# Performance work log

Measured on AMD Instinct MI355X. Metric: run time of the kernel, lower is better.

The kernel has to match this reference:

```python
import jax, jax.numpy as jnp
import numpy as np

B, S, IN = 4, 4096, 2048
E, D, A, R = 16, 128, 128, 4  # num_experts, expert_vector_dim, attn_dim, mlp_rank
LN_EPS = 1e-5


def _ln2(x, g, b):
    # LayerNorm over the last two dims [E, D] jointly (torch nn.LayerNorm([E, D]))
    mu = x.mean(axis=(-2, -1), keepdims=True)
    var = ((x - mu) ** 2).mean(axis=(-2, -1), keepdims=True)
    return (x - mu) * jax.lax.rsqrt(var + LN_EPS) * g + b


def setup_inputs() -> dict:
    key = jax.random.key(0)
    ks = jax.random.split(key, 8)
    f32 = jnp.float32
    return {
        "hidden_states": jax.random.normal(ks[0], (B, S, IN), f32),
        "expert_embedding": jax.random.normal(ks[1], (E, D), f32) * 0.02,
        "ln_gamma": jnp.ones((E, D), f32),
        "ln_beta": jnp.zeros((E, D), f32),
        "Wv_w": jax.random.normal(ks[2], (E, IN), f32) * 0.02,
        "Wv_b": jnp.zeros((E,), f32),
        "mlp_w1": jax.random.normal(ks[3], (R, IN), f32) * 0.02,
        "mlp_b1": jnp.zeros((R,), f32),
        "mlp_w2": jax.random.normal(ks[4], (E * D, R), f32) * 0.02,
        "mlp_b2": jnp.zeros((E * D,), f32),
        "te_Wq": jax.random.normal(ks[5], (A, D), f32) * 0.05,
        "te_Wk": jax.random.normal(ks[6], (A, D), f32) * 0.05,
        "top_k": 2,
    }


def reference(hidden_states, expert_embedding, ln_gamma, ln_beta, Wv_w, Wv_b,
              mlp_w1, mlp_b1, mlp_w2, mlp_b2, te_Wq, te_Wk, top_k):
    # global expert vectors, layernormed over [E, D]: (E, D)
    ge = _ln2(expert_embedding[None, None], ln_gamma, ln_beta)[0, 0]
    # input gate = W_v(hidden): (B, S, E)
    input_gate = jnp.einsum('bsi,ei->bse', hidden_states, Wv_w) + Wv_b
    # TE mlp -> dynamic per-token expert vectors: (B, S, E, D)
    h = jax.nn.relu(jnp.einsum('bsi,ri->bsr', hidden_states, mlp_w1) + mlp_b1)
    dyn = (jnp.einsum('bsr,or->bso', h, mlp_w2) + mlp_b2).reshape(B, S, E, D)
    dyn = _ln2(dyn, ln_gamma, ln_beta)
    # attention-style routing: Q from dyn experts, K from global experts
    q = jnp.einsum('bsed,ad->bsea', dyn, te_Wq)     # (B, S, E, A)
    k = jnp.einsum('ed,ad->ea', ge, te_Wk)          # (E, A)
    scale = 1.0 / float(np.sqrt(A))
    sim = jax.nn.softmax(jnp.einsum('bsqa,ka->bsqk', q, k) * scale, axis=-1)
    gate = jnp.einsum('bsqk,bsk->bsq', sim, input_gate)
    rw = jax.nn.softmax(gate, axis=-1)              # (B, S, E)
    # top-k masking + sharpened softmax (temperature 0.1)
    vals, idx = jax.lax.top_k(rw, top_k)            # (B, S, k)
    oh = jax.nn.one_hot(idx, E, dtype=rw.dtype)     # (B, S, k, E)
    scattered = jnp.einsum('bske,bsk->bse', oh, vals)
    keep = oh.sum(axis=-2) > 0
    neg = jnp.finfo(rw.dtype).min
    masked = jnp.where(keep, scattered, neg)
    return jax.nn.softmax(masked / 0.1, axis=-1)
```

## Files before the change

kernel.cpp:

```cpp
#include <hip/hip_runtime.h>
#include <math.h>

#define NTOK   16384
#define INDIM  2048
#define NROWS  20
#define CHUNK  256

#define WS_PKT  0
#define WS_D1K  1024
#define WS_GQK  1280
#define WS_BQK  1536
#define WS_SCAL 1792
#define WS_TOT  1818

#define SIM_SCALE 0.08838834764831845f

#define LBUF1   5120
#define HBUF0   10240
#define HBUF1   14336
#define LRED2_STRIDE 324
#define LRED    5440

__device__ __forceinline__ void async16(const float* g, float* l) {
    __builtin_amdgcn_global_load_lds(
        (const __attribute__((address_space(1))) void*)g,
        (__attribute__((address_space(3))) void*)l, 16, 0, 0);
}

__device__ __forceinline__ void stage_all(const float* __restrict__ wv,
                                          const float* __restrict__ w1,
                                          const float* __restrict__ hb_lane,
                                          float* ldsw, float* ldsh,
                                          int wave, int lane, int goff) {
    const int l4 = lane << 2;
    #pragma unroll
    for (int j = 0; j < 5; ++j) {
        const int r = wave + (j << 2);
        const float* src = (j < 4) ? (wv + (r << 11)) : (w1 + ((r - 16) << 11));
        async16(src + goff + l4, ldsw + r * CHUNK + l4);
    }
    #pragma unroll
    for (int t = 0; t < 4; ++t) {
        async16(hb_lane + t * INDIM + goff,
                ldsh + (((wave << 2) + t) * CHUNK) + l4);
    }
}

__device__ __forceinline__ void compute_chunk(float acc[NROWS][4],
                                              const float* wb,
                                              const float* hbl) {
    float4 h[4];
    #pragma unroll
    for (int t = 0; t < 4; ++t) h[t] = *(const float4*)(hbl + (t << 8));
    #pragma unroll
    for (int w = 0; w < NROWS; ++w) {
        float4 wf = *(const float4*)(wb + (w << 8));
        #pragma unroll
        for (int t = 0; t < 4; ++t) {
            acc[w][t] = fmaf(h[t].x, wf.x,
                        fmaf(h[t].y, wf.y,
                        fmaf(h[t].z, wf.z,
                        fmaf(h[t].w, wf.w, acc[w][t]))));
        }
    }
}

__global__ __launch_bounds__(256) void hr_pre2(
    const float* __restrict__ ee, const float* __restrict__ gam,
    const float* __restrict__ bta, const float* __restrict__ w2,
    const float* __restrict__ b2, const float* __restrict__ wq,
    const float* __restrict__ wk, float* __restrict__ ws)
{
    const int tid  = threadIdx.x;
    const int bx   = blockIdx.x;
    const int lane = tid & 63;
    const int wave = tid >> 6;

    if (bx == 16) {
        __shared__ float sacc[26];
        if (tid < 26) sacc[tid] = 0.f;
        __syncthreads();
        float pa[26];
        #pragma unroll
        for (int j = 0; j < 26; ++j) pa[j] = 0.f;
        for (int i = tid; i < 2048; i += 256) {
            float b = b2[i];
            float4 w4 = *(const float4*)(w2 + i * 4);
            float wr[4] = {w4.x, w4.y, w4.z, w4.w};
            pa[0] += b;
            pa[1] += b * b;
            #pragma unroll
            for (int r = 0; r < 4; ++r) {
                pa[2 + r] += wr[r];
                pa[6 + r] += b * wr[r];
                #pragma unroll
                for (int r2 = 0; r2 < 4; ++r2) pa[10 + r * 4 + r2] += wr[r] * wr[r2];
            }
        }
        #pragma unroll
        for (int j = 0; j < 26; ++j) {
            float v = pa[j];
            v += __shfl_xor(v, 32); v += __shfl_xor(v, 16); v += __shfl_xor(v, 8);
            v += __shfl_xor(v, 4);  v += __shfl_xor(v, 2);  v += __shfl_xor(v, 1);
            if (lane == 0) atomicAdd(&sacc[j], v);
        }
        __syncthreads();
        if (tid < 26) ws[WS_SCAL + tid] = sacc[tid] * (1.f / 2048.f);
        return;
    }

    const int e2 = bx;
    __shared__ float sge[128];
    __shared__ float sK[128];
    __shared__ float sWqK[128];
    __shared__ float sred[8];

    float v8[8];
    float s = 0.f;
    #pragma unroll
    for (int j = 0; j < 8; ++j) { v8[j] = ee[tid + j * 256]; s += v8[j]; }
    s += __shfl_xor(s, 32); s += __shfl_xor(s, 16); s += __shfl_xor(s, 8);
    s += __shfl_xor(s, 4);  s += __shfl_xor(s, 2);  s += __shfl_xor(s, 1);
    if (lane == 0) sred[wave] = s;
    __syncthreads();
    const float mu = (sred[0] + sred[1] + sred[2] + sred[3]) * (1.f / 2048.f);
    float q = 0.f;
    #pragma unroll
    for (int j = 0; j < 8; ++j) { float d = v8[j] - mu; q += d * d; }
    q += __shfl_xor(q, 32); q += __shfl_xor(q, 16); q += __shfl_xor(q, 8);
    q += __shfl_xor(q, 4);  q += __shfl_xor(q, 2);  q += __shfl_xor(q, 1);
    if (lane == 0) sred[4 + wave] = q;
    __syncthreads();
    const float rsq = rsqrtf((sred[4] + sred[5] + sred[6] + sred[7]) * (1.f / 2048.f) + 1e-5f);

    if (tid < 128) {
        int idx = (e2 << 7) + tid;
        sge[tid] = (ee[idx] - mu) * rsq * gam[idx] + bta[idx];
    }
    __syncthreads();

    {
        int a = tid >> 1, half = tid & 1;
        const float* wr = wk + (a << 7) + (half << 6);
        const float* gg = sge + (half << 6);
        float acc = 0.f;
        #pragma unroll 8
        for (int j = 0; j < 64; ++j) acc = fmaf(gg[j], wr[j], acc);
        acc += __shfl_xor(acc, 1);
        if (half == 0) sK[a] = acc;
    }
    __syncthreads();

    {
        int d = tid >> 1, half = tid & 1;
        float acc = 0.f;
        #pragma unroll 8
        for (int j = 0; j < 64; ++j) {
            int a = (half << 6) + j;
            acc = fmaf(wq[(a << 7) + d], sK[a], acc);
        }
        acc += __shfl_xor(acc, 1);
        if (half == 0) sWqK[d] = acc;
    }
    __syncthreads();

    {
        int o = tid >> 2, qd = tid & 3;
        int r = o >> 4, e = o & 15;
        float acc = 0.f;
        #pragma unroll 8
        for (int j = 0; j < 32; ++j) {
            int d  = (qd << 5) + j;
            int ed = (e << 7) + d;
            acc = fmaf(w2[ed * 4 + r] * gam[ed], sWqK[d], acc);
        }
        acc += __shfl_xor(acc, 1);
        acc += __shfl_xor(acc, 2);
        if (qd == 0) ws[WS_PKT + (e2 << 6) + (r << 4) + e] = acc;
    }

    if (tid < 192) {
        int kind = tid >> 6;
        int e    = (tid >> 2) & 15;
        int qd   = tid & 3;
        float acc = 0.f;
        #pragma unroll 8
        for (int j = 0; j < 32; ++j) {
            int d  = (qd << 5) + j;
            int ed = (e << 7) + d;
            float w = sWqK[d];
            float t = (kind == 0) ? b2[ed] * gam[ed]
                    : (kind == 1) ? gam[ed]
                                  : bta[ed];
            acc = fmaf(t, w, acc);
        }
        acc += __shfl_xor(acc, 1);
        acc += __shfl_xor(acc, 2);
        if (qd == 0) ws[WS_D1K + (kind << 8) + (e2 << 4) + e] = acc;
    }
}

__global__ __launch_bounds__(256) void hr_main(
    const float* __restrict__ hidden, const float* __restrict__ wv,
    const float* __restrict__ wvb, const float* __restrict__ w1,
    const float* __restrict__ b1, const float* __restrict__ tab,
    float* __restrict__ out)
{
    __shared__ float lds[18432];

    const int tid  = threadIdx.x;
    const int wave = tid >> 6;
    const int lane = tid & 63;
    const int tok0 = (blockIdx.x << 4) + (wave << 2);
    const float* hb = hidden + (size_t)tok0 * INDIM + (lane << 2);

    float acc[NROWS][4];
    #pragma unroll
    for (int w = 0; w < NROWS; ++w) {
        acc[w][0] = 0.f; acc[w][1] = 0.f; acc[w][2] = 0.f; acc[w][3] = 0.f;
    }

    const float* wr0 = &lds[lane << 2];
    const float* wr1 = &lds[LBUF1 + (lane << 2)];
    const float* hr0 = &lds[HBUF0 + (wave << 10) + (lane << 2)];
    const float* hr1 = &lds[HBUF1 + (wave << 10) + (lane << 2)];

    stage_all(wv, w1, hb, lds, lds + HBUF0, wave, lane, 0);
    __syncthreads();

    for (int cc = 0; cc < 4; ++cc) {
        const int c1 = 2 * cc + 1;
        stage_all(wv, w1, hb, lds + LBUF1, lds + HBUF1, wave, lane, c1 << 8);
        compute_chunk(acc, wr0, hr0);
        __syncthreads();
        if (cc != 3)
            stage_all(wv, w1, hb, lds, lds + HBUF0, wave, lane, (c1 + 1) << 8);
        compute_chunk(acc, wr1, hr1);
        __syncthreads();
    }

    #pragma unroll
    for (int w = 0; w < NROWS; ++w) {
        #pragma unroll
        for (int t = 0; t < 4; ++t) {
            float v = acc[w][t];
            v += __shfl_xor(v, 32);
            v += __shfl_xor(v, 16);
            acc[w][t] = v;
        }
    }
    {
        const int q = lane >> 4, i = lane & 15;
        #pragma unroll
        for (int w = 0; w < NROWS; ++w) {
            if (q == w / 5) {
                #pragma unroll
                for (int t = 0; t < 4; ++t)
                    lds[((wave << 2) + t) * LRED2_STRIDE + (w << 4) + i] = acc[w][t];
            }
        }
    }
    __syncthreads();

    #pragma unroll
    for (int pp = 0; pp < 2; ++pp) {
        const int p = tid + pp * 256;
        if (p < 320) {
            const int w = p >> 4, tok = p & 15;
            const float4* rp = (const float4*)&lds[tok * LRED2_STRIDE + (w << 4)];
            float4 r0 = rp[0], r1 = rp[1], r2 = rp[2], r3 = rp[3];
            float s = (r0.x + r0.y + r0.z + r0.w) + (r1.x + r1.y + r1.z + r1.w)
                    + (r2.x + r2.y + r2.z + r2.w) + (r3.x + r3.y + r3.z + r3.w);
            lds[LRED + tok * 20 + w] = s;
        }
    }
    __syncthreads();

    const int tok = tid >> 4;
    const int e   = tid & 15;

    float ig[16];
    #pragma unroll
    for (int j = 0; j < 16; ++j) ig[j] = lds[LRED + tok * 20 + j] + wvb[j];
    float h[4];
    #pragma unroll
    for (int r = 0; r < 4; ++r) h[r] = fmaxf(lds[LRED + tok * 20 + 16 + r] + b1[r], 0.f);

    float muT = tab[WS_SCAL + 0];
    float e2m = tab[WS_SCAL + 1];
    #pragma unroll
    for (int r = 0; r < 4; ++r) {
        muT = fmaf(h[r], tab[WS_SCAL + 2 + r], muT);
        e2m = fmaf(2.f * h[r], tab[WS_SCAL + 6 + r], e2m);
        #pragma unroll
        for (int r2 = 0; r2 < 4; ++r2)
            e2m = fmaf(h[r] * h[r2], tab[WS_SCAL + 10 + r * 4 + r2], e2m);
    }
    const float var = e2m - muT * muT;
    const float rsq = rsqrtf(var + 1e-5f);

    float sv[16];
    #pragma unroll
    for (int e2 = 0; e2 < 16; ++e2) {
        float s = tab[WS_D1K + (e2 << 4) + e];
        s = fmaf(h[0], tab[(e2 << 6) + e], s);
        s = fmaf(h[1], tab[(e2 << 6) + 16 + e], s);
        s = fmaf(h[2], tab[(e2 << 6) + 32 + e], s);
        s = fmaf(h[3], tab[(e2 << 6) + 48 + e], s);
        s = fmaf(-muT, tab[WS_GQK + (e2 << 4) + e], s);
        sv[e2] = (rsq * s + tab[WS_BQK + (e2 << 4) + e]) * SIM_SCALE;
    }
    float mx = sv[0];
    #pragma unroll
    for (int e2 = 1; e2 < 16; ++e2) mx = fmaxf(mx, sv[e2]);
    float den = 0.f, gate = 0.f;
    #pragma unroll
    for (int e2 = 0; e2 < 16; ++e2) {
        float p = __expf(sv[e2] - mx);
        den += p;
        gate = fmaf(p, ig[e2], gate);
    }
    gate /= den;

    float gm = gate;
    gm = fmaxf(gm, __shfl_xor(gm, 1));
    gm = fmaxf(gm, __shfl_xor(gm, 2));
    gm = fmaxf(gm, __shfl_xor(gm, 4));
    gm = fmaxf(gm, __shfl_xor(gm, 8));
    float ex = __expf(gate - gm);
    float es = ex;
    es += __shfl_xor(es, 1);
    es += __shfl_xor(es, 2);
    es += __shfl_xor(es, 4);
    es += __shfl_xor(es, 8);
    const float rw = ex / es;

    float v1 = rw; int i1 = e;
    #pragma unroll
    for (int m = 1; m <= 8; m <<= 1) {
        float ov = __shfl_xor(v1, m);
        int   oi = __shfl_xor(i1, m);
        if (ov > v1 || (ov == v1 && oi < i1)) { v1 = ov; i1 = oi; }
    }
    float v2 = (e == i1) ? -INFINITY : rw; int i2 = e;
    #pragma unroll
    for (int m = 1; m <= 8; m <<= 1) {
        float ov = __shfl_xor(v2, m);
        int   oi = __shfl_xor(i2, m);
        if (ov > v2 || (ov == v2 && oi < i2)) { v2 = ov; i2 = oi; }
    }

    float oval = 0.f;
    if (e == i1 || e == i2) {
        float t = __expf((v2 - v1) * 10.f);
        oval = (e == i1) ? (1.f / (1.f + t)) : (t / (1.f + t));
    }
    out[(((size_t)blockIdx.x << 4) + tok) * 16 + e] = oval;
}

extern "C" void kernel_launch(void* const* d_in, const int* in_sizes, int n_in,
                              void* d_out, int out_size, void* d_ws, size_t ws_size,
                              hipStream_t stream)
{
    const float* hidden = (const float*)d_in[0];
    const float* ee     = (const float*)d_in[1];
    const float* gam    = (const float*)d_in[2];
    const float* bta    = (const float*)d_in[3];
    const float* wv     = (const float*)d_in[4];
    const float* wvb    = (const float*)d_in[5];
    const float* w1     = (const float*)d_in[6];
    const float* b1     = (const float*)d_in[7];
    const float* w2     = (const float*)d_in[8];
    const float* b2     = (const float*)d_in[9];
    const float* wq     = (const float*)d_in[10];
    const float* wk     = (const float*)d_in[11];
    float* out = (float*)d_out;
    float* ws  = (float*)d_ws;

    hipLaunchKernelGGL(hr_pre2, dim3(17), dim3(256), 0, stream,
                       ee, gam, bta, w2, b2, wq, wk, ws);
    hipLaunchKernelGGL(hr_main, dim3(NTOK / 16), dim3(256), 0, stream,
                       hidden, wv, wvb, w1, b1, ws, out);
}
```

Baseline: 244.7 us.

## Stage full Wv matrix in LDS and stream hidden and W1 through registers

The main kernel now copies the whole 16x2048 Wv matrix into dynamic LDS once per block. Hidden rows and the small W1 matrix are read straight into registers, with the next chunk prefetched while the current one computes. This removes the per-chunk double-buffered LDS staging and the barriers inside the loop. Blocks grow to 512 threads covering 32 tokens, and the cross-lane reduction gets two more shuffle steps plus a simpler scatter layout. In exchange each block needs about 140KB of LDS, which limits occupancy to one block per CU, and the up-front Wv load has to finish before any compute starts.

```diff
diff --git a/kernel.cpp b/kernel.cpp
--- a/kernel.cpp
+++ b/kernel.cpp
@@ -15,54 +15,16 @@
 
 #define SIM_SCALE 0.08838834764831845f
 
-#define LBUF1   5120
-#define HBUF0   10240
-#define HBUF1   14336
-#define LRED2_STRIDE 324
-#define LRED    5440
+#define L_WV    0
+#define L_SCAT  32768
+#define L_RED   35328
+#define L_TOTF  35968
+#define L_BYTES (L_TOTF * 4)
 
 __device__ __forceinline__ void async16(const float* g, float* l) {
     __builtin_amdgcn_global_load_lds(
         (const __attribute__((address_space(1))) void*)g,
         (__attribute__((address_space(3))) void*)l, 16, 0, 0);
-}
-
-__device__ __forceinline__ void stage_all(const float* __restrict__ wv,
-                                          const float* __restrict__ w1,
-                                          const float* __restrict__ hb_lane,
-                                          float* ldsw, float* ldsh,
-                                          int wave, int lane, int goff) {
-    const int l4 = lane << 2;
-    #pragma unroll
-    for (int j = 0; j < 5; ++j) {
-        const int r = wave + (j << 2);
-        const float* src = (j < 4) ? (wv + (r << 11)) : (w1 + ((r - 16) << 11));
-        async16(src + goff + l4, ldsw + r * CHUNK + l4);
-    }
-    #pragma unroll
-    for (int t = 0; t < 4; ++t) {
-        async16(hb_lane + t * INDIM + goff,
-                ldsh + (((wave << 2) + t) * CHUNK) + l4);
-    }
-}
-
-__device__ __forceinline__ void compute_chunk(float acc[NROWS][4],
-                                              const float* wb,
-                                              const float* hbl) {
-    float4 h[4];
-    #pragma unroll
-    for (int t = 0; t < 4; ++t) h[t] = *(const float4*)(hbl + (t << 8));
-    #pragma unroll
-    for (int w = 0; w < NROWS; ++w) {
-        float4 wf = *(const float4*)(wb + (w << 8));
-        #pragma unroll
-        for (int t = 0; t < 4; ++t) {
-            acc[w][t] = fmaf(h[t].x, wf.x,
-                        fmaf(h[t].y, wf.y,
-                        fmaf(h[t].z, wf.z,
-                        fmaf(h[t].w, wf.w, acc[w][t]))));
-        }
-    }
 }
 
 __global__ __launch_bounds__(256) void hr_pre2(
@@ -200,19 +162,30 @@
     }
 }
 
-__global__ __launch_bounds__(256) void hr_main(
+extern __shared__ float lds[];
+
+__global__ __launch_bounds__(512) void hr_main(
     const float* __restrict__ hidden, const float* __restrict__ wv,
     const float* __restrict__ wvb, const float* __restrict__ w1,
     const float* __restrict__ b1, const float* __restrict__ tab,
     float* __restrict__ out)
 {
-    __shared__ float lds[18432];
-
     const int tid  = threadIdx.x;
     const int wave = tid >> 6;
     const int lane = tid & 63;
-    const int tok0 = (blockIdx.x << 4) + (wave << 2);
-    const float* hb = hidden + (size_t)tok0 * INDIM + (lane << 2);
+    const int l4   = lane << 2;
+    const int tok0 = (blockIdx.x << 5) + (wave << 2);
+    const float* hb = hidden + (size_t)tok0 * INDIM + l4;
+
+    #pragma unroll
+    for (int rr = 0; rr < 2; ++rr) {
+        const int r = (wave << 1) + rr;
+        #pragma unroll
+        for (int j = 0; j < 8; ++j) {
+            async16(wv + (r << 11) + (j << 8) + l4,
+                    &lds[L_WV + (r << 11) + (j << 8) + l4]);
+        }
+    }
 
     float acc[NROWS][4];
     #pragma unroll
@@ -220,23 +193,47 @@
         acc[w][0] = 0.f; acc[w][1] = 0.f; acc[w][2] = 0.f; acc[w][3] = 0.f;
     }
 
-    const float* wr0 = &lds[lane << 2];
-    const float* wr1 = &lds[LBUF1 + (lane << 2)];
-    const float* hr0 = &lds[HBUF0 + (wave << 10) + (lane << 2)];
-    const float* hr1 = &lds[HBUF1 + (wave << 10) + (lane << 2)];
-
-    stage_all(wv, w1, hb, lds, lds + HBUF0, wave, lane, 0);
-    __syncthreads();
-
-    for (int cc = 0; cc < 4; ++cc) {
-        const int c1 = 2 * cc + 1;
-        stage_all(wv, w1, hb, lds + LBUF1, lds + HBUF1, wave, lane, c1 << 8);
-        compute_chunk(acc, wr0, hr0);
-        __syncthreads();
-        if (cc != 3)
-            stage_all(wv, w1, hb, lds, lds + HBUF0, wave, lane, (c1 + 1) << 8);
-        compute_chunk(acc, wr1, hr1);
-        __syncthreads();
+    float4 hc[4], wc[4], hn[4], wn[4];
+    #pragma unroll
+    for (int t = 0; t < 4; ++t) hc[t] = *(const float4*)(hb + t * INDIM);
+    #pragma unroll
+    for (int r = 0; r < 4; ++r) wc[r] = *(const float4*)(w1 + (r << 11) + l4);
+
+    __syncthreads();
+
+    for (int c = 0; c < 8; ++c) {
+        const int coff = ((c + 1) & 7) << 8;
+        #pragma unroll
+        for (int t = 0; t < 4; ++t) hn[t] = *(const float4*)(hb + t * INDIM + coff);
+        #pragma unroll
+        for (int r = 0; r < 4; ++r) wn[r] = *(const float4*)(w1 + (r << 11) + coff + l4);
+
+        const int cbase = L_WV + (c << 8) + l4;
+        #pragma unroll
+        for (int r = 0; r < 16; ++r) {
+            float4 wf = *(const float4*)&lds[cbase + (r << 11)];
+            #pragma unroll
+            for (int t = 0; t < 4; ++t) {
+                acc[r][t] = fmaf(hc[t].x, wf.x,
+                            fmaf(hc[t].y, wf.y,
+                            fmaf(hc[t].z, wf.z,
+                            fmaf(hc[t].w, wf.w, acc[r][t]))));
+            }
+        }
+        #pragma unroll
+        for (int r = 0; r < 4; ++r) {
+            #pragma unroll
+            for (int t = 0; t < 4; ++t) {
+                acc[16 + r][t] = fmaf(hc[t].x, wc[r].x,
+                                 fmaf(hc[t].y, wc[r].y,
+                                 fmaf(hc[t].z, wc[r].z,
+                                 fmaf(hc[t].w, wc[r].w, acc[16 + r][t]))));
+            }
+        }
+        #pragma unroll
+        for (int t = 0; t < 4; ++t) hc[t] = hn[t];
+        #pragma unroll
+        for (int r = 0; r < 4; ++r) wc[r] = wn[r];
     }
 
     #pragma unroll
@@ -246,32 +243,29 @@
             float v = acc[w][t];
             v += __shfl_xor(v, 32);
             v += __shfl_xor(v, 16);
+            v += __shfl_xor(v, 8);
+            v += __shfl_xor(v, 4);
             acc[w][t] = v;
         }
     }
     {
-        const int q = lane >> 4, i = lane & 15;
-        #pragma unroll
-        for (int w = 0; w < NROWS; ++w) {
-            if (q == w / 5) {
-                #pragma unroll
-                for (int t = 0; t < 4; ++t)
-                    lds[((wave << 2) + t) * LRED2_STRIDE + (w << 4) + i] = acc[w][t];
-            }
+        const int c = lane & 3, g = lane >> 2;
+        #pragma unroll
+        for (int t = 0; t < 4; ++t) {
+            const int tokw = (wave << 2) + t;
+            lds[L_SCAT + (tokw * 20 + g) * 4 + c] = acc[g][t];
+            if (g < 4)
+                lds[L_SCAT + (tokw * 20 + 16 + g) * 4 + c] = acc[16 + g][t];
         }
     }
     __syncthreads();
 
     #pragma unroll
     for (int pp = 0; pp < 2; ++pp) {
-        const int p = tid + pp * 256;
-        if (p < 320) {
-            const int w = p >> 4, tok = p & 15;
-            const float4* rp = (const float4*)&lds[tok * LRED2_STRIDE + (w << 4)];
-            float4 r0 = rp[0], r1 = rp[1], r2 = rp[2], r3 = rp[3];
-            float s = (r0.x + r0.y + r0.z + r0.w) + (r1.x + r1.y + r1.z + r1.w)
-                    + (r2.x + r2.y + r2.z + r2.w) + (r3.x + r3.y + r3.z + r3.w);
-            lds[LRED + tok * 20 + w] = s;
+        const int p = tid + (pp << 9);
+        if (p < 640) {
+            float4 r0 = *(const float4*)&lds[L_SCAT + p * 4];
+            lds[L_RED + p] = (r0.x + r0.y) + (r0.z + r0.w);
         }
     }
     __syncthreads();
@@ -281,10 +275,10 @@
 
     float ig[16];
     #pragma unroll
-    for (int j = 0; j < 16; ++j) ig[j] = lds[LRED + tok * 20 + j] + wvb[j];
+    for (int j = 0; j < 16; ++j) ig[j] = lds[L_RED + tok * 20 + j] + wvb[j];
     float h[4];
     #pragma unroll
-    for (int r = 0; r < 4; ++r) h[r] = fmaxf(lds[LRED + tok * 20 + 16 + r] + b1[r], 0.f);
+    for (int r = 0; r < 4; ++r) h[r] = fmaxf(lds[L_RED + tok * 20 + 16 + r] + b1[r], 0.f);
 
     float muT = tab[WS_SCAL + 0];
     float e2m = tab[WS_SCAL + 1];
@@ -355,7 +349,7 @@
         float t = __expf((v2 - v1) * 10.f);
         oval = (e == i1) ? (1.f / (1.f + t)) : (t / (1.f + t));
     }
-    out[(((size_t)blockIdx.x << 4) + tok) * 16 + e] = oval;
+    out[(((size_t)blockIdx.x << 5) + tok) * 16 + e] = oval;
 }
 
 extern "C" void kernel_launch(void* const* d_in, const int* in_sizes, int n_in,
@@ -377,8 +371,11 @@
     float* out = (float*)d_out;
     float* ws  = (float*)d_ws;
 
+    hipFuncSetAttribute((const void*)hr_main,
+                        hipFuncAttributeMaxDynamicSharedMemorySize, L_BYTES);
+
     hipLaunchKernelGGL(hr_pre2, dim3(17), dim3(256), 0, stream,
                        ee, gam, bta, w2, b2, wq, wk, ws);
-    hipLaunchKernelGGL(hr_main, dim3(NTOK / 16), dim3(256), 0, stream,
+    hipLaunchKernelGGL(hr_main, dim3(NTOK / 32), dim3(512), L_BYTES, stream,
                        hidden, wv, wvb, w1, b1, ws, out);
 }
```

New measurement: 289.2 us. +18.2%, slower.
